# Kernel tuning notes

Hardware: AMD Instinct MI355X
Metric: run time of the kernel (lower is better)

Reference implementation:

```python
import jax, jax.numpy as jnp
import numpy as np
import math

H = 512      # d_model
N = 64       # d_state
B = 16
L = 4096
DT_MIN, DT_MAX = 0.001, 0.1


def setup_inputs() -> dict:
    key = jax.random.key(0)
    ks = jax.random.split(key, 6)
    u = jax.random.normal(ks[0], (B, H, L), dtype=jnp.float32)
    # S4DKernel parameters
    C = jax.random.normal(ks[1], (H, N // 2, 2), dtype=jnp.float32)  # view_as_real of cfloat C
    log_dt = (jax.random.uniform(ks[2], (H,), dtype=jnp.float32)
              * (math.log(DT_MAX) - math.log(DT_MIN)) + math.log(DT_MIN))
    log_A_real = jnp.log(0.5 * jnp.ones((H, N // 2), dtype=jnp.float32))
    A_imag = math.pi * jnp.broadcast_to(jnp.arange(N // 2, dtype=jnp.float32), (H, N // 2))
    # S4D parameters
    D = jax.random.normal(ks[3], (H,), dtype=jnp.float32)
    # output_linear: Conv1d(H, 2H, kernel_size=1) -> weight (2H, H), bias (2H,)
    W = jax.random.normal(ks[4], (2 * H, H), dtype=jnp.float32) * (1.0 / math.sqrt(H))
    b = jax.random.normal(ks[5], (2 * H,), dtype=jnp.float32) * 0.01
    return {"u": u, "C": C, "log_dt": log_dt, "log_A_real": log_A_real,
            "A_imag": A_imag, "D": D, "W": W, "b": b}


def _s4d_kernel(C, log_dt, log_A_real, A_imag, L):
    """Generate the (H, L) convolution kernel from diagonal SSM parameters."""
    dt = jnp.exp(log_dt)                                    # (H,)
    Cc = C[..., 0] + 1j * C[..., 1]                         # (H, N/2) complex
    A = -jnp.exp(log_A_real) + 1j * A_imag                  # (H, N/2)
    dtA = A * dt[:, None]                                   # (H, N/2)
    # Vandermonde: exp(dtA * l) for l in [0, L)
    K = jnp.exp(dtA[:, :, None] * jnp.arange(L, dtype=jnp.float32))  # (H, N/2, L)
    Cw = Cc * (jnp.exp(dtA) - 1.0) / A                      # (H, N/2)
    k = 2.0 * jnp.einsum('hn,hnl->hl', Cw, K).real          # (H, L)
    return k


def reference(u, C, log_dt, log_A_real, A_imag, D, W, b):
    Lc = u.shape[-1]
    k = _s4d_kernel(C, log_dt, log_A_real, A_imag, Lc)      # (H, L)
    # FFT long convolution (linear conv via zero-padding to 2L)
    k_f = jnp.fft.rfft(k, n=2 * Lc)                          # (H, L+1)
    u_f = jnp.fft.rfft(u, n=2 * Lc)                          # (B, H, L+1)
    y = jnp.fft.irfft(u_f * k_f, n=2 * Lc)[..., :Lc]         # (B, H, L)
    y = y + u * D[:, None]
    y = jax.nn.gelu(y, approximate=False)                    # torch nn.GELU default
    # output_linear: 1x1 Conv1d (H -> 2H) then GLU over channel dim
    z = jnp.einsum('oh,bhl->bol', W, y) + b[None, :, None]   # (B, 2H, L)
    a, g = jnp.split(z, 2, axis=1)
    return a * jax.nn.sigmoid(g)                             # (B, H, L)
```

## Files before the change

kernel.cpp:

```cpp
#include <hip/hip_runtime.h>

#define BB 16
#define HH 512
#define NH 32
#define LL 4096
#define TCH 64
#define NCH 64
#define KA 128

static_assert(TCH * NCH == LL, "chunking");

typedef __attribute__((ext_vector_type(8))) short bf16x8;
typedef __attribute__((ext_vector_type(4))) float f32x4;

static __device__ __forceinline__ unsigned short f2bf(float x) {
    return __builtin_bit_cast(unsigned short, (__bf16)x);
}
static __device__ __forceinline__ float bf2f(unsigned short b) {
    return __builtin_bit_cast(float, ((unsigned)b) << 16);
}
static __device__ __forceinline__ unsigned pack2(float a, float b) {
    return (unsigned)f2bf(a) | ((unsigned)f2bf(b) << 16);
}

static __device__ __forceinline__ void gload_lds16(const void* g, void* l) {
#if __has_builtin(__builtin_amdgcn_global_load_lds)
    __builtin_amdgcn_global_load_lds(
        (const __attribute__((address_space(1))) unsigned int*)g,
        (__attribute__((address_space(3))) unsigned int*)l, 16, 0, 0);
#else
    *(uint4*)l = *(const uint4*)g;
#endif
}

__global__ void k0_params(const float* __restrict__ C,
                          const float* __restrict__ log_dt,
                          const float* __restrict__ lAr,
                          const float* __restrict__ Aim,
                          float* __restrict__ c2R,  float* __restrict__ c2I,
                          float* __restrict__ ltR,  float* __restrict__ ltI,
                          float* __restrict__ xrA,  float* __restrict__ xiA)
{
    int tid = blockIdx.x * 256 + threadIdx.x;
    if (tid >= HH * NH) return;
    int h = tid >> 5;
    float dt = expf(log_dt[h]);
    float Ar = -expf(lAr[tid]);
    float Ai = Aim[tid];
    float xr = Ar * dt, xi = Ai * dt;
    xrA[tid] = xr; xiA[tid] = xi;
    float er = expf(xr);
    float lr = er * cosf(xi);
    float li = er * sinf(xi);
    float wr = lr - 1.0f, wi = li;
    float inv = 1.0f / (Ar * Ar + Ai * Ai);
    float qr = (wr * Ar + wi * Ai) * inv;
    float qi = (wi * Ar - wr * Ai) * inv;
    float cr = C[2 * tid], ci = C[2 * tid + 1];
    c2R[tid] =  2.0f * (cr * qr - ci * qi);
    c2I[tid] = -2.0f * (cr * qi + ci * qr);
    float eT = expf((float)TCH * xr);
    float aT = (float)TCH * xi;
    ltR[tid] = eT * cosf(aT);
    ltI[tid] = eT * sinf(aT);
}

__global__ void kw_pack(const float* __restrict__ W, const float* __restrict__ bias,
                        unsigned short* __restrict__ Wp, float* __restrict__ bp)
{
    int tid = blockIdx.x * 256 + threadIdx.x;
    int drow = tid >> 6;
    int kc = (tid & 63) * 8;
    int src = (drow & 1) ? (drow >> 1) + HH : (drow >> 1);
    const float4* s = (const float4*)(W + (size_t)src * HH + kc);
    float4 a = s[0], b4 = s[1];
    uint4 pack;
    pack.x = pack2(a.x, a.y);
    pack.y = pack2(a.z, a.w);
    pack.z = pack2(b4.x, b4.y);
    pack.w = pack2(b4.z, b4.w);
    *(uint4*)(Wp + (size_t)drow * HH + kc) = pack;
    if (tid < 2 * HH)
        bp[tid] = bias[(tid & 1) ? (tid >> 1) + HH : (tid >> 1)];
}

__global__ __launch_bounds__(64) void kA_build(
    const float* __restrict__ c2R, const float* __restrict__ c2I,
    const float* __restrict__ xrA, const float* __restrict__ xiA,
    const float* __restrict__ Dv,
    unsigned short* __restrict__ Apan, unsigned short* __restrict__ Vpan)
{
    int h = blockIdx.x;
    int t = threadIdx.x;
    __shared__ float s_xr[NH], s_xi[NH], s_cr[NH], s_ci[NH], s_k[TCH];
    if (t < NH) {
        s_xr[t] = xrA[h * NH + t]; s_xi[t] = xiA[h * NH + t];
        s_cr[t] = c2R[h * NH + t]; s_ci[t] = c2I[h * NH + t];
    }
    __syncthreads();
    {
        float d = (float)t;
        float acc = 0.f;
#pragma unroll
        for (int n = 0; n < NH; ++n) {
            float er = __expf(s_xr[n] * d);
            float sv, cv; __sincosf(s_xi[n] * d, &sv, &cv);
            acc = fmaf(s_cr[n], er * cv, fmaf(s_ci[n], er * sv, acc));
        }
        s_k[t] = acc;
    }
    __syncthreads();
    float k0d = s_k[0] + Dv[h];
    unsigned short row[KA];
#pragma unroll
    for (int tau = 0; tau < TCH; ++tau)
        row[tau] = f2bf((tau < t) ? s_k[t - tau] : (tau == t ? k0d : 0.f));
    float tp = (float)(t + 1);
#pragma unroll
    for (int n = 0; n < NH; ++n) {
        float er = __expf(s_xr[n] * tp);
        float sv, cv; __sincosf(s_xi[n] * tp, &sv, &cv);
        float pr = er * cv, pi = er * sv;
        row[TCH + 2 * n]     = f2bf(fmaf(s_cr[n], pr,  s_ci[n] * pi));
        row[TCH + 2 * n + 1] = f2bf(fmaf(s_ci[n], pr, -s_cr[n] * pi));
    }
    {
        uint4* dst = (uint4*)(Apan + ((size_t)h * TCH + t) * KA);
        const uint4* src = (const uint4*)row;
#pragma unroll
        for (int i = 0; i < 16; ++i) dst[i] = src[i];
    }
    {
        int n = t >> 1, cm = t & 1;
        float xr = s_xr[n], xi = s_xi[n];
        unsigned short vrow[TCH];
#pragma unroll
        for (int tau = 0; tau < TCH; ++tau) {
            float p = (float)(TCH - 1 - tau);
            float er = __expf(xr * p);
            float sv, cv; __sincosf(xi * p, &sv, &cv);
            vrow[tau] = f2bf(cm ? er * sv : er * cv);
        }
        uint4* vd = (uint4*)(Vpan + ((size_t)h * TCH + t) * TCH);
        const uint4* vs = (const uint4*)vrow;
#pragma unroll
        for (int i = 0; i < 8; ++i) vd[i] = vs[i];
    }
}

__global__ __launch_bounds__(256, 4) void kBCD(
    const float* __restrict__ u,
    const unsigned short* __restrict__ Apan, const unsigned short* __restrict__ Vpan,
    const float* __restrict__ ltR, const float* __restrict__ ltI,
    unsigned short* __restrict__ yb)
{
    __shared__ unsigned short Sl[4][TCH * TCH];
    int h = blockIdx.x & (HH - 1), g = blockIdx.x >> 9;
    int tid = threadIdx.x;
    int lane = tid & 63, w = tid >> 6;
    int b = g * 4 + w;
    int lrow = lane & 15, hi = lane >> 4, lk8 = hi * 8;
    const float* ug = u + ((size_t)b * HH + h) * LL;
    const unsigned short* Ap = Apan + (size_t)h * TCH * KA;
    const unsigned short* Vp = Vpan + (size_t)h * TCH * TCH;
    char* Sw = (char*)Sl[w];

    bf16x8 ub[2][4];
#pragma unroll
    for (int ks = 0; ks < 2; ++ks)
#pragma unroll
        for (int n = 0; n < 4; ++n) {
            int c = n * 16 + lrow;
            const float* up = ug + c * TCH + ks * 32 + lk8;
            float4 f0 = *(const float4*)up, f1 = *(const float4*)(up + 4);
            bf16x8 v;
            v[0]=f2bf(f0.x); v[1]=f2bf(f0.y); v[2]=f2bf(f0.z); v[3]=f2bf(f0.w);
            v[4]=f2bf(f1.x); v[5]=f2bf(f1.y); v[6]=f2bf(f1.z); v[7]=f2bf(f1.w);
            ub[ks][n] = v;
        }

    f32x4 accE[4][4];
#pragma unroll
    for (int m = 0; m < 4; ++m)
#pragma unroll
        for (int n = 0; n < 4; ++n) { f32x4 z = {0.f,0.f,0.f,0.f}; accE[m][n] = z; }
#pragma unroll
    for (int ks = 0; ks < 2; ++ks) {
        bf16x8 vf[4];
#pragma unroll
        for (int m = 0; m < 4; ++m)
            vf[m] = *(const bf16x8*)(Vp + (m * 16 + lrow) * TCH + ks * 32 + lk8);
#pragma unroll
        for (int m = 0; m < 4; ++m)
#pragma unroll
            for (int n = 0; n < 4; ++n)
                accE[m][n] = __builtin_amdgcn_mfma_f32_16x16x32_bf16(vf[m], ub[ks][n], accE[m][n], 0, 0, 0);
    }
#pragma unroll
    for (int m = 0; m < 4; ++m) {
        int j0 = m * 16 + hi * 4;
#pragma unroll
        for (int n = 0; n < 4; ++n) {
            int c = n * 16 + lrow;
            f32x4 v = accE[m][n];
            uint2 p; p.x = pack2(v[0], v[1]); p.y = pack2(v[2], v[3]);
            *(uint2*)(Sw + c * 128 + ((2 * j0) ^ ((c & 7) << 4))) = p;
        }
    }
    asm volatile("s_waitcnt lgkmcnt(0)" ::: "memory");

    if (lane < NH) {
        int n = lane;
        float ar = ltR[h * NH + n], ai = ltI[h * NH + n];
        unsigned ev[NCH];
#pragma unroll
        for (int c = 0; c < NCH; ++c)
            ev[c] = *(const unsigned*)(Sw + c * 128 + ((4 * n) ^ ((c & 7) << 4)));
        float sr = 0.f, si = 0.f;
#pragma unroll
        for (int c = 0; c < NCH; ++c) {
            *(unsigned*)(Sw + c * 128 + ((4 * n) ^ ((c & 7) << 4))) = pack2(sr, si);
            float er = bf2f((unsigned short)(ev[c] & 0xffffu));
            float ei = bf2f((unsigned short)(ev[c] >> 16));
            float nsr = fmaf(ar, sr, fmaf(-ai, si, er));
            float nsi = fmaf(ar, si, fmaf(ai, sr, ei));
            sr = nsr; si = nsi;
        }
    }
    asm volatile("s_waitcnt lgkmcnt(0)" ::: "memory");

    f32x4 acc[4][4];
#pragma unroll
    for (int m = 0; m < 4; ++m)
#pragma unroll
        for (int n = 0; n < 4; ++n) { f32x4 z = {0.f,0.f,0.f,0.f}; acc[m][n] = z; }
#pragma unroll
    for (int ks = 0; ks < 2; ++ks) {
        bf16x8 af[4];
#pragma unroll
        for (int m = 0; m < 4; ++m)
            af[m] = *(const bf16x8*)(Ap + (m * 16 + lrow) * KA + ks * 32 + lk8);
#pragma unroll
        for (int m = 0; m < 4; ++m)
#pragma unroll
            for (int n = 0; n < 4; ++n)
                acc[m][n] = __builtin_amdgcn_mfma_f32_16x16x32_bf16(af[m], ub[ks][n], acc[m][n], 0, 0, 0);
    }
#pragma unroll
    for (int ks = 2; ks < 4; ++ks) {
        bf16x8 af[4], bfr[4];
#pragma unroll
        for (int m = 0; m < 4; ++m)
            af[m] = *(const bf16x8*)(Ap + (m * 16 + lrow) * KA + ks * 32 + lk8);
#pragma unroll
        for (int n = 0; n < 4; ++n) {
            int c = n * 16 + lrow;
            int bo = (ks - 2) * 64 + lk8 * 2;
            bfr[n] = *(const bf16x8*)(Sw + c * 128 + (bo ^ ((c & 7) << 4)));
        }
#pragma unroll
        for (int m = 0; m < 4; ++m)
#pragma unroll
            for (int n = 0; n < 4; ++n)
                acc[m][n] = __builtin_amdgcn_mfma_f32_16x16x32_bf16(af[m], bfr[n], acc[m][n], 0, 0, 0);
    }
    unsigned short* yrow = yb + ((size_t)b * HH + h) * LL;
#pragma unroll
    for (int m = 0; m < 4; ++m) {
        int t0 = m * 16 + hi * 4;
#pragma unroll
        for (int n = 0; n < 4; ++n) {
            int c = n * 16 + lrow;
            f32x4 v = acc[m][n];
            unsigned short o[4];
#pragma unroll
            for (int r = 0; r < 4; ++r) {
                float yo = v[r];
                float ge = 0.5f * yo * (1.0f + erff(yo * 0.70710678118f));
                o[r] = f2bf(ge);
            }
            uint2 pw;
            pw.x = (unsigned)o[0] | ((unsigned)o[1] << 16);
            pw.y = (unsigned)o[2] | ((unsigned)o[3] << 16);
            *(uint2*)(yrow + c * TCH + t0) = pw;
        }
    }
}

__global__ __launch_bounds__(256) void kT_transpose(
    const unsigned short* __restrict__ yb, unsigned short* __restrict__ yt)
{
    __shared__ unsigned short T[64][130];
    int bid = blockIdx.x;
    int lt = bid & 31;
    int ht = (bid >> 5) & 7;
    int b  = bid >> 8;
    int t = threadIdx.x;
#pragma unroll
    for (int r = 0; r < 4; ++r) {
        int chunk = r * 256 + t;
        int row = chunk >> 4;
        int c16 = chunk & 15;
        uint4 v = *(const uint4*)(yb + ((size_t)(b * HH + ht * 64 + row)) * LL
                                     + lt * 128 + c16 * 8);
        *(uint4*)&T[row][c16 * 8] = v;
    }
    __syncthreads();
    int oct = t & 7, lgrp = t >> 3;
    size_t obase = ((size_t)b * LL + (size_t)lt * 128) * HH + ht * 64 + oct * 8;
#pragma unroll
    for (int r = 0; r < 2; ++r) {
        int l = (r * 32 + lgrp) * 2;
        unsigned v[8];
#pragma unroll
        for (int k = 0; k < 8; ++k)
            v[k] = *(const unsigned*)&T[oct * 8 + k][l];
        uint4 w0, w1;
        w0.x = (v[0] & 0xffffu) | (v[1] << 16);
        w0.y = (v[2] & 0xffffu) | (v[3] << 16);
        w0.z = (v[4] & 0xffffu) | (v[5] << 16);
        w0.w = (v[6] & 0xffffu) | (v[7] << 16);
        w1.x = (v[0] >> 16) | (v[1] & 0xffff0000u);
        w1.y = (v[2] >> 16) | (v[3] & 0xffff0000u);
        w1.z = (v[4] >> 16) | (v[5] & 0xffff0000u);
        w1.w = (v[6] >> 16) | (v[7] & 0xffff0000u);
        *(uint4*)(yt + obase + (size_t)l * HH) = w0;
        *(uint4*)(yt + obase + (size_t)(l + 1) * HH) = w1;
    }
}

#define BM 128
#define BN 128
#define BKK 32

__global__ __launch_bounds__(256, 2) void k4_gemm(
    const unsigned short* __restrict__ Wp, const float* __restrict__ bp,
    const unsigned short* __restrict__ yt, float* __restrict__ out)
{
    __shared__ unsigned short As[BM * BKK];
    __shared__ unsigned short Bs[BN * BKK];
    int tid  = threadIdx.x;
    int bidx = blockIdx.x;
    int mtile = bidx & 7, ntile = bidx >> 3;
    int mbase = mtile * BM, nbase = ntile * BN;
    int lane = tid & 63;
    int wv = tid >> 6;
    int wr = wv >> 1, wc = wv & 1;
    int lrow = lane & 15;
    int lk = (lane >> 4) * 8;

    f32x4 acc[4][4];
#pragma unroll
    for (int m = 0; m < 4; ++m)
#pragma unroll
        for (int n = 0; n < 4; ++n) { f32x4 z = {0.f,0.f,0.f,0.f}; acc[m][n] = z; }

    for (int kk = 0; kk < HH; kk += BKK) {
#pragma unroll
        for (int p = 0; p < 2; ++p) {
            int chunk = p * 256 + tid;
            int row = chunk >> 2;
            int kc  = (chunk & 3) * 8;
            gload_lds16(Wp + (size_t)(mbase + row) * HH + kk + kc, &As[chunk * 8]);
            gload_lds16(yt + (size_t)(nbase + row) * HH + kk + kc, &Bs[chunk * 8]);
        }
        __syncthreads();
        bf16x8 af[4], bfr[4];
#pragma unroll
        for (int m = 0; m < 4; ++m)
            af[m] = *(const bf16x8*)&As[(wr * 64 + m * 16 + lrow) * BKK + lk];
#pragma unroll
        for (int nf = 0; nf < 4; ++nf)
            bfr[nf] = *(const bf16x8*)&Bs[(wc * 64 + nf * 16 + lrow) * BKK + lk];
#pragma unroll
        for (int m = 0; m < 4; ++m)
#pragma unroll
            for (int nf = 0; nf < 4; ++nf)
                acc[m][nf] = __builtin_amdgcn_mfma_f32_16x16x32_bf16(af[m], bfr[nf], acc[m][nf], 0, 0, 0);
        __syncthreads();
    }
#pragma unroll
    for (int m = 0; m < 4; ++m) {
        int go = mbase + wr * 64 + m * 16 + ((lane >> 4) * 4);
        float4 bv = *(const float4*)(bp + go);
#pragma unroll
        for (int nf = 0; nf < 4; ++nf) {
            int col  = nbase + wc * 64 + nf * 16 + lrow;
            int bcol = col >> 12;
            int lcol = col & (LL - 1);
            f32x4 v = acc[m][nf];
            float a0 = v[0] + bv.x, g0 = v[1] + bv.y;
            float a1 = v[2] + bv.z, g1 = v[3] + bv.w;
            float o0 = a0 / (1.0f + __expf(-g0));
            float o1 = a1 / (1.0f + __expf(-g1));
            size_t ob = ((size_t)bcol * HH + (size_t)(go >> 1)) * LL + lcol;
            out[ob] = o0;
            out[ob + LL] = o1;
        }
    }
}

extern "C" void kernel_launch(void* const* d_in, const int* in_sizes, int n_in,
                              void* d_out, int out_size, void* d_ws, size_t ws_size,
                              hipStream_t stream) {
    const float* u    = (const float*)d_in[0];
    const float* C    = (const float*)d_in[1];
    const float* ldt  = (const float*)d_in[2];
    const float* lar  = (const float*)d_in[3];
    const float* aim  = (const float*)d_in[4];
    const float* Dv   = (const float*)d_in[5];
    const float* W    = (const float*)d_in[6];
    const float* bias = (const float*)d_in[7];
    float* out = (float*)d_out;

    char* w = (char*)d_ws;
    float* c2R = (float*)w; w += (size_t)HH * NH * 4;
    float* c2I = (float*)w; w += (size_t)HH * NH * 4;
    float* ltR = (float*)w; w += (size_t)HH * NH * 4;
    float* ltI = (float*)w; w += (size_t)HH * NH * 4;
    float* xrA = (float*)w; w += (size_t)HH * NH * 4;
    float* xiA = (float*)w; w += (size_t)HH * NH * 4;
    float* bp  = (float*)w; w += (size_t)2 * HH * 4;
    unsigned short* Wp   = (unsigned short*)w; w += (size_t)2 * HH * HH * 2;
    unsigned short* Apan = (unsigned short*)w; w += (size_t)HH * TCH * KA * 2;
    unsigned short* Vpan = (unsigned short*)w; w += (size_t)HH * TCH * TCH * 2;
    unsigned short* yt   = (unsigned short*)w; w += (size_t)BB * LL * HH * 2;

    unsigned short* yb = (unsigned short*)d_out;

    k0_params   <<<dim3(64),   dim3(256), 0, stream>>>(C, ldt, lar, aim, c2R, c2I, ltR, ltI, xrA, xiA);
    kw_pack     <<<dim3(256),  dim3(256), 0, stream>>>(W, bias, Wp, bp);
    kA_build    <<<dim3(512),  dim3(64),  0, stream>>>(c2R, c2I, xrA, xiA, Dv, Apan, Vpan);
    kBCD        <<<dim3(2048), dim3(256), 0, stream>>>(u, Apan, Vpan, ltR, ltI, yb);
    kT_transpose<<<dim3(4096), dim3(256), 0, stream>>>(yb, yt);
    k4_gemm     <<<dim3(4096), dim3(256), 0, stream>>>(Wp, bp, yt, out);
}
```

Baseline: 215.8 us.

## Restructure kBCD MFMA loops per m-tile to cut register pressure

The MFMA accumulation in kBCD now runs one 16-row m-tile at a time, keeping 4 accumulators live instead of 16, and the GELU epilogue is fused into each m-tile pass. The serial chunk scan loads its 64 LDS values in groups of 8 rather than all at once. Occupancy is pinned with amdgpu_waves_per_eu(4,4). The goal is fewer VGPRs so the kernel can hold occupancy without spilling, at the cost of reloading B fragments from LDS per m-tile and less instruction-level parallelism.

```diff
diff --git a/kernel.cpp b/kernel.cpp
--- a/kernel.cpp
+++ b/kernel.cpp
@@ -148,7 +148,9 @@
     }
 }
 
-__global__ __launch_bounds__(256, 4) void kBCD(
+__global__ __launch_bounds__(256)
+__attribute__((amdgpu_waves_per_eu(4, 4)))
+void kBCD(
     const float* __restrict__ u,
     const unsigned short* __restrict__ Apan, const unsigned short* __restrict__ Vpan,
     const float* __restrict__ ltR, const float* __restrict__ ltI,
@@ -179,31 +181,23 @@
             ub[ks][n] = v;
         }
 
-    f32x4 accE[4][4];
-#pragma unroll
-    for (int m = 0; m < 4; ++m)
-#pragma unroll
-        for (int n = 0; n < 4; ++n) { f32x4 z = {0.f,0.f,0.f,0.f}; accE[m][n] = z; }
-#pragma unroll
-    for (int ks = 0; ks < 2; ++ks) {
-        bf16x8 vf[4];
-#pragma unroll
-        for (int m = 0; m < 4; ++m)
-            vf[m] = *(const bf16x8*)(Vp + (m * 16 + lrow) * TCH + ks * 32 + lk8);
-#pragma unroll
-        for (int m = 0; m < 4; ++m)
+#pragma unroll
+    for (int m = 0; m < 4; ++m) {
+        f32x4 accE[4];
+#pragma unroll
+        for (int n = 0; n < 4; ++n) { f32x4 z = {0.f,0.f,0.f,0.f}; accE[n] = z; }
+#pragma unroll
+        for (int ks = 0; ks < 2; ++ks) {
+            bf16x8 vf = *(const bf16x8*)(Vp + (m * 16 + lrow) * TCH + ks * 32 + lk8);
 #pragma unroll
             for (int n = 0; n < 4; ++n)
-                accE[m][n] = __builtin_amdgcn_mfma_f32_16x16x32_bf16(vf[m], ub[ks][n], accE[m][n], 0, 0, 0);
-    }
-#pragma unroll
-    for (int m = 0; m < 4; ++m) {
+                accE[n] = __builtin_amdgcn_mfma_f32_16x16x32_bf16(vf, ub[ks][n], accE[n], 0, 0, 0);
+        }
         int j0 = m * 16 + hi * 4;
 #pragma unroll
         for (int n = 0; n < 4; ++n) {
             int c = n * 16 + lrow;
-            f32x4 v = accE[m][n];
-            uint2 p; p.x = pack2(v[0], v[1]); p.y = pack2(v[2], v[3]);
+            uint2 p; p.x = pack2(accE[n][0], accE[n][1]); p.y = pack2(accE[n][2], accE[n][3]);
             *(uint2*)(Sw + c * 128 + ((2 * j0) ^ ((c & 7) << 4))) = p;
         }
     }
@@ -212,66 +206,54 @@
     if (lane < NH) {
         int n = lane;
         float ar = ltR[h * NH + n], ai = ltI[h * NH + n];
-        unsigned ev[NCH];
-#pragma unroll
-        for (int c = 0; c < NCH; ++c)
-            ev[c] = *(const unsigned*)(Sw + c * 128 + ((4 * n) ^ ((c & 7) << 4)));
         float sr = 0.f, si = 0.f;
 #pragma unroll
-        for (int c = 0; c < NCH; ++c) {
-            *(unsigned*)(Sw + c * 128 + ((4 * n) ^ ((c & 7) << 4))) = pack2(sr, si);
-            float er = bf2f((unsigned short)(ev[c] & 0xffffu));
-            float ei = bf2f((unsigned short)(ev[c] >> 16));
-            float nsr = fmaf(ar, sr, fmaf(-ai, si, er));
-            float nsi = fmaf(ar, si, fmaf(ai, sr, ei));
-            sr = nsr; si = nsi;
+        for (int gg = 0; gg < 8; ++gg) {
+            unsigned ev[8];
+#pragma unroll
+            for (int k = 0; k < 8; ++k)
+                ev[k] = *(const unsigned*)(Sw + (gg * 8 + k) * 128 + ((4 * n) ^ (k << 4)));
+#pragma unroll
+            for (int k = 0; k < 8; ++k) {
+                *(unsigned*)(Sw + (gg * 8 + k) * 128 + ((4 * n) ^ (k << 4))) = pack2(sr, si);
+                float er = bf2f((unsigned short)(ev[k] & 0xffffu));
+                float ei = bf2f((unsigned short)(ev[k] >> 16));
+                float nsr = fmaf(ar, sr, fmaf(-ai, si, er));
+                float nsi = fmaf(ar, si, fmaf(ai, sr, ei));
+                sr = nsr; si = nsi;
+            }
         }
     }
     asm volatile("s_waitcnt lgkmcnt(0)" ::: "memory");
 
-    f32x4 acc[4][4];
-#pragma unroll
-    for (int m = 0; m < 4; ++m)
-#pragma unroll
-        for (int n = 0; n < 4; ++n) { f32x4 z = {0.f,0.f,0.f,0.f}; acc[m][n] = z; }
-#pragma unroll
-    for (int ks = 0; ks < 2; ++ks) {
-        bf16x8 af[4];
-#pragma unroll
-        for (int m = 0; m < 4; ++m)
-            af[m] = *(const bf16x8*)(Ap + (m * 16 + lrow) * KA + ks * 32 + lk8);
-#pragma unroll
-        for (int m = 0; m < 4; ++m)
+    unsigned short* yrow = yb + ((size_t)b * HH + h) * LL;
+#pragma unroll
+    for (int m = 0; m < 4; ++m) {
+        f32x4 acc[4];
+#pragma unroll
+        for (int n = 0; n < 4; ++n) { f32x4 z = {0.f,0.f,0.f,0.f}; acc[n] = z; }
+#pragma unroll
+        for (int ks = 0; ks < 2; ++ks) {
+            bf16x8 af = *(const bf16x8*)(Ap + (m * 16 + lrow) * KA + ks * 32 + lk8);
 #pragma unroll
             for (int n = 0; n < 4; ++n)
-                acc[m][n] = __builtin_amdgcn_mfma_f32_16x16x32_bf16(af[m], ub[ks][n], acc[m][n], 0, 0, 0);
-    }
-#pragma unroll
-    for (int ks = 2; ks < 4; ++ks) {
-        bf16x8 af[4], bfr[4];
-#pragma unroll
-        for (int m = 0; m < 4; ++m)
-            af[m] = *(const bf16x8*)(Ap + (m * 16 + lrow) * KA + ks * 32 + lk8);
+                acc[n] = __builtin_amdgcn_mfma_f32_16x16x32_bf16(af, ub[ks][n], acc[n], 0, 0, 0);
+        }
+#pragma unroll
+        for (int ks = 0; ks < 2; ++ks) {
+            bf16x8 af = *(const bf16x8*)(Ap + (m * 16 + lrow) * KA + 64 + ks * 32 + lk8);
+#pragma unroll
+            for (int n = 0; n < 4; ++n) {
+                int c = n * 16 + lrow;
+                bf16x8 bfr = *(const bf16x8*)(Sw + c * 128 + ((ks * 64 + lk8 * 2) ^ ((c & 7) << 4)));
+                acc[n] = __builtin_amdgcn_mfma_f32_16x16x32_bf16(af, bfr, acc[n], 0, 0, 0);
+            }
+        }
+        int t0 = m * 16 + hi * 4;
 #pragma unroll
         for (int n = 0; n < 4; ++n) {
             int c = n * 16 + lrow;
-            int bo = (ks - 2) * 64 + lk8 * 2;
-            bfr[n] = *(const bf16x8*)(Sw + c * 128 + (bo ^ ((c & 7) << 4)));
-        }
-#pragma unroll
-        for (int m = 0; m < 4; ++m)
-#pragma unroll
-            for (int n = 0; n < 4; ++n)
-                acc[m][n] = __builtin_amdgcn_mfma_f32_16x16x32_bf16(af[m], bfr[n], acc[m][n], 0, 0, 0);
-    }
-    unsigned short* yrow = yb + ((size_t)b * HH + h) * LL;
-#pragma unroll
-    for (int m = 0; m < 4; ++m) {
-        int t0 = m * 16 + hi * 4;
-#pragma unroll
-        for (int n = 0; n < 4; ++n) {
-            int c = n * 16 + lrow;
-            f32x4 v = acc[m][n];
+            f32x4 v = acc[n];
             unsigned short o[4];
 #pragma unroll
             for (int r = 0; r < 4; ++r) {
```

After: 220.9 us. 1.02x slower.
